# Kernel optimization log

Measured on AMD Instinct MI355X. Metric: run time of the kernel, lower is better.

The kernel has to match this reference:

```python
import jax, jax.numpy as jnp
import numpy as np

B, V, D, K, C_IN, C_OUT = 64, 2000, 16, 3, 64, 64


def setup_inputs() -> dict:
    key = jax.random.key(0)
    ks = jax.random.split(key, 7)
    return {
        "x": jax.random.normal(ks[0], (B, V, C_IN), dtype=jnp.float32),
        "ne_re": jax.random.normal(ks[1], (V, D), dtype=jnp.float32),
        "ne_im": jax.random.normal(ks[2], (V, D), dtype=jnp.float32),
        "w_re": jax.random.normal(ks[3], (D, K, C_IN, C_OUT), dtype=jnp.float32),
        "w_im": jax.random.normal(ks[4], (D, K, C_IN, C_OUT), dtype=jnp.float32),
        "b_re": jax.random.normal(ks[5], (D, C_OUT), dtype=jnp.float32),
        "b_im": jax.random.normal(ks[6], (D, C_OUT), dtype=jnp.float32),
    }


def reference(x, ne_re, ne_im, w_re, w_im, b_re, b_im):
    # Complex node embeddings and parameter pools (param_type='complex').
    ne = jax.lax.complex(ne_re, ne_im)                      # (V, D) complex64
    w_pool = jax.lax.complex(w_re, w_im)                    # (D, K, Ci, Co)
    b_pool = jax.lax.complex(b_re, b_im)                    # (D, Co)

    # Laplacian = E E^H, Frobenius-normalized (activation=None, normalization='frob').
    lap = ne @ ne.conj().T                                  # (V, V)
    lap = lap / jnp.linalg.norm(lap)

    # Node-adaptive weights and bias.
    weights = jnp.einsum('vd,dkio->vkio', ne, w_pool)       # (V, K, Ci, Co)
    bias = ne @ b_pool                                      # (V, Co)

    # Chebyshev-style recurrence, faithful to the source: T_k = 2*T_{k-1} - T_{k-2}
    # (the original code omits the laplacian matmul in the recurrence).
    polys = [jnp.eye(V, dtype=lap.dtype), lap]
    for k in range(2, K):
        polys.append(2.0 * polys[k - 1] - polys[k - 2])
    cheb = jnp.stack(polys, axis=0)                         # (K, V, V)

    xc = x.astype(lap.dtype)                                # (B, V, Ci)
    gx = jnp.einsum('kuv,bvi->buki', cheb, xc)              # (B, V, K, Ci)
    out = jnp.einsum('bvki,vkio->bvo', gx, weights) + bias  # (B, V, Co) complex

    # unwind=True path: view_as_real + flatten(2,3) -> interleaved (re, im).
    return jnp.stack([out.real, out.imag], axis=-1).reshape(B, V, 2 * C_OUT)
```

## Files before the change

### kernel.cpp

```cpp
#include <hip/hip_runtime.h>
#include <stdint.h>

#define BB 64
#define VV 2000
#define DD 16
#define CI 64
#define CO 64

#define WS_INV_DW   0
#define WS_GRAM_DW  8
#define WS_Z_DW     1024
#define WS_BIAS_DW  132096
#define WS_NE_B     1552384UL
#define WS_RHS_B    1814528UL
#define WS_U_B      4960256UL
#define WS_W_B      54112256UL
#define WS_ZP_DW    (WS_W_B / 4)

typedef __attribute__((ext_vector_type(8))) short short8;
typedef __attribute__((ext_vector_type(4))) float f32x4;

__device__ __forceinline__ uint32_t f2bf(float f) {
  uint32_t u = __float_as_uint(f);
  return (u + 0x7FFFu + ((u >> 16) & 1u)) >> 16;
}

__global__ void k_zero(float* __restrict__ ws) {
  reinterpret_cast<float4*>(ws)[threadIdx.x] = make_float4(0.f, 0.f, 0.f, 0.f);
}

__global__ void k_ne(const float* __restrict__ ne_re, const float* __restrict__ ne_im,
                     float* __restrict__ ws) {
  int gid = blockIdx.x * 256 + threadIdx.x;
  int u = gid >> 6, col = gid & 63;
  int h = col >> 5, kk = col & 31, d = kk >> 1, p = kk & 1;
  float v = 0.f;
  if (u < VV) v = p ? ne_im[u*DD + d] : ne_re[u*DD + d];
  uint32_t hi = f2bf(v);
  uint32_t ov = h ? f2bf(v - __uint_as_float(hi << 16)) : hi;
  ((uint16_t*)((char*)ws + WS_NE_B))[gid] = (uint16_t)ov;
}

__global__ void k_rhs(const float* __restrict__ w_re, const float* __restrict__ w_im,
                      float* __restrict__ ws) {
  int bx = blockIdx.x;
  int c = bx >> 4, ig4 = bx & 15;
  int t = threadIdx.x;
  int o = t & 63, il = t >> 6;
  int i = ig4*4 + il;
  int cb = c >> 1;
  int imf = c & 1;

  uint32_t row32[16];
  #pragma unroll
  for (int d = 0; d < DD; ++d) {
    int b0 = (d*192 + i)*64 + o;
    float vre, vim;
    if (cb == 0) {
      vre = w_re[b0] - w_re[b0 + 8192];
      vim = w_im[b0] - w_im[b0 + 8192];
    } else {
      vre = w_re[b0 + 4096] + 2.f*w_re[b0 + 8192];
      vim = w_im[b0 + 4096] + 2.f*w_im[b0 + 8192];
    }
    float q0 = imf ? vim : vre;
    float q1 = imf ? vre : -vim;
    row32[d] = f2bf(q0) | (f2bf(q1) << 16);
  }
  int s = ((i >> 3) ^ (o & 7)) & 7;
  int n = c*4096 + o*64 + s*8 + (i & 7);
  uint4* dst = (uint4*)((uint16_t*)((char*)ws + WS_RHS_B) + (size_t)n*64);
  #pragma unroll
  for (int j = 0; j < 4; ++j) {
    uint4 qv = make_uint4(row32[4*j], row32[4*j+1], row32[4*j+2], row32[4*j+3]);
    dst[j]     = qv;
    dst[j + 4] = qv;
  }
}

__global__ void k_norm1(const float* __restrict__ ne_re, const float* __restrict__ ne_im,
                        float* __restrict__ ws) {
  int t = threadIdx.x;
  int d = t >> 4, e = t & 15;
  int v0 = blockIdx.x * 80;
  float gr = 0.f, gi = 0.f;
  for (int v = v0; v < v0 + 80; ++v) {
    float ar = ne_re[v*DD + d], ai = ne_im[v*DD + d];
    float br = ne_re[v*DD + e], bi = ne_im[v*DD + e];
    gr += ar*br + ai*bi;
    gi += ar*bi - ai*br;
  }
  atomicAdd(ws + WS_GRAM_DW + 2*t,     gr);
  atomicAdd(ws + WS_GRAM_DW + 2*t + 1, gi);
}

__global__ void k_norm2(float* __restrict__ ws) {
  int t = threadIdx.x;
  float gr = ws[WS_GRAM_DW + 2*t], gi = ws[WS_GRAM_DW + 2*t + 1];
  __shared__ float red[256];
  red[t] = gr*gr + gi*gi;
  __syncthreads();
  for (int k = 128; k > 0; k >>= 1) {
    if (t < k) red[t] += red[t + k];
    __syncthreads();
  }
  if (t == 0) ws[WS_INV_DW] = 1.0f / sqrtf(red[0]);
}

__global__ void k_bias(const float* __restrict__ ne_re, const float* __restrict__ ne_im,
                       const float* __restrict__ b_re, const float* __restrict__ b_im,
                       float* __restrict__ ws) {
  int gid = blockIdx.x * 256 + threadIdx.x;
  int u = gid >> 7, idx = gid & 127;
  int o = idx >> 1, half = idx & 1;
  float acc = 0.f;
  #pragma unroll
  for (int d = 0; d < DD; ++d) {
    float nr = ne_re[u*DD + d], ni = ne_im[u*DD + d];
    float pr = b_re[d*CO + o],  pi = b_im[d*CO + o];
    acc += half ? (nr*pi + ni*pr) : (nr*pr - ni*pi);
  }
  ws[WS_BIAS_DW + gid] = acc;
}

__global__ void __launch_bounds__(256, 4)
k_z(const float* __restrict__ x, const float* __restrict__ ne_re,
    const float* __restrict__ ne_im, float* __restrict__ ws) {
  int b = blockIdx.x >> 4, c = blockIdx.x & 15;
  int t = threadIdx.x, lane = t & 63;
  int w = __builtin_amdgcn_readfirstlane(t >> 6);
  __shared__ __align__(16) float smem[8192];

  int vbase = c * 125;

  {
    const float4* xg = (const float4*)(x + ((size_t)b * VV + vbase) * CI);
    float4 rx[8];
    #pragma unroll
    for (int p = 0; p < 8; ++p) {
      int idx = p * 256 + t;
      if (idx < 2000) rx[p] = xg[idx];
    }
    #pragma unroll
    for (int p = 0; p < 8; ++p) {
      int idx = p * 256 + t;
      if (idx < 2000) *(float4*)&smem[idx * 4] = rx[p];
    }
  }
  __syncthreads();

  float zr[DD], zi[DD];
  #pragma unroll
  for (int d = 0; d < DD; ++d) { zr[d] = 0.f; zi[d] = 0.f; }

  int lv0 = (w * 125) >> 2;
  int lv1 = ((w + 1) * 125) >> 2;
  #pragma unroll 4
  for (int lv = lv0; lv < lv1; ++lv) {
    float xv = smem[lv * 64 + lane];
    int v = vbase + lv;
    #pragma unroll
    for (int d = 0; d < DD; ++d) {
      zr[d] += ne_re[v*DD + d] * xv;
      zi[d] -= ne_im[v*DD + d] * xv;
    }
  }
  __syncthreads();

  #pragma unroll
  for (int d = 0; d < DD; ++d) {
    smem[w*2048 + d*128 + lane*2 + 0] = zr[d];
    smem[w*2048 + d*128 + lane*2 + 1] = zi[d];
  }
  __syncthreads();
  float* ZP = ws + WS_ZP_DW;
  #pragma unroll
  for (int k = 0; k < 8; ++k) {
    int j = t + k*256;
    float s = smem[j] + smem[2048 + j] + smem[4096 + j] + smem[6144 + j];
    int d = j >> 7, r = j & 127;
    ZP[(size_t)c*131072 + d*8192 + b*128 + r] = s;
  }
}

__global__ void k_zred(float* __restrict__ ws) {
  int g = blockIdx.x * 256 + threadIdx.x;
  const float2* ZP2 = (const float2*)(ws + WS_ZP_DW);
  float2 acc = make_float2(0.f, 0.f);
  #pragma unroll
  for (int c = 0; c < 16; ++c) {
    float2 v = ZP2[(size_t)c*65536 + g];
    acc.x += v.x; acc.y += v.y;
  }
  ((float2*)(ws + WS_Z_DW))[g] = acc;
}

__global__ void __launch_bounds__(256, 4)
k_wgemm(float* __restrict__ ws) {
  const uint16_t* NE  = (const uint16_t*)((char*)ws + WS_NE_B);
  const uint16_t* RHS = (const uint16_t*)((char*)ws + WS_RHS_B);
  uint32_t*       W   = (uint32_t*)((char*)ws + WS_W_B);
  int ut = blockIdx.x, nc = blockIdx.y;
  int t = threadIdx.x, w = t >> 6, lane = t & 63;
  int n16 = lane & 15, quad = lane >> 4;
  short8 a[4][2];
  #pragma unroll
  for (int m = 0; m < 4; ++m) {
    int u = ut*64 + m*16 + n16;
    a[m][0] = *(const short8*)(NE + u*64 + quad*8);
    a[m][1] = *(const short8*)(NE + u*64 + 32 + quad*8);
  }
  int nbase = nc*1024 + w*256;
  #pragma unroll 2
  for (int pt = 0; pt < 8; ++pt) {
    int nb = nbase + pt*32;
    const uint16_t* r0 = RHS + (size_t)(nb + 2*n16 + 0)*64 + quad*8;
    const uint16_t* r1 = RHS + (size_t)(nb + 2*n16 + 1)*64 + quad*8;
    short8 b00 = *(const short8*)r0;
    short8 b01 = *(const short8*)(r0 + 32);
    short8 b10 = *(const short8*)r1;
    short8 b11 = *(const short8*)(r1 + 32);
    #pragma unroll
    for (int m = 0; m < 4; ++m) {
      f32x4 acc0 = (f32x4){0.f,0.f,0.f,0.f};
      f32x4 acc1 = (f32x4){0.f,0.f,0.f,0.f};
      acc0 = __builtin_amdgcn_mfma_f32_16x16x32_bf16(a[m][0], b00, acc0, 0, 0, 0);
      acc0 = __builtin_amdgcn_mfma_f32_16x16x32_bf16(a[m][1], b01, acc0, 0, 0, 0);
      acc1 = __builtin_amdgcn_mfma_f32_16x16x32_bf16(a[m][0], b10, acc1, 0, 0, 0);
      acc1 = __builtin_amdgcn_mfma_f32_16x16x32_bf16(a[m][1], b11, acc1, 0, 0, 0);
      #pragma unroll
      for (int r = 0; r < 4; ++r) {
        int u = ut*64 + m*16 + quad*4 + r;
        if (u < VV) {
          uint32_t pk = f2bf(acc0[r]) | (f2bf(acc1[r]) << 16);
          W[(size_t)u*8192 + (nb >> 1) + n16] = pk;
        }
      }
    }
  }
}

__global__ void __launch_bounds__(256, 4)
k_u(const float* __restrict__ x, const float* __restrict__ ne_re,
    const float* __restrict__ ne_im, float* __restrict__ ws) {
  int ug = blockIdx.x, by = blockIdx.y;
  int t = threadIdx.x, q = t >> 6, i = t & 63;
  int b = by*4 + q;
  float invn = ws[WS_INV_DW];

  float xv[16];
  {
    const float* xp = x + ((size_t)b*VV + (size_t)ug*16)*CI + i;
    #pragma unroll
    for (int ul = 0; ul < 16; ++ul) xv[ul] = xp[(size_t)ul*CI];
  }

  const float* Z = ws + WS_Z_DW;
  float zr[DD], zi[DD];
  #pragma unroll
  for (int d = 0; d < DD; ++d) {
    const float* zp = Z + (size_t)(d*4096 + b*64 + i) * 2;
    zr[d] = zp[0]; zi[d] = zp[1];
  }

  __shared__ uint16_t sStage[192 * 64];
  int bkey = b & 7;
  int pos = (((i >> 3) ^ bkey) & 7)*8 + (i & 7);

  #pragma unroll
  for (int ul = 0; ul < 16; ++ul)
    sStage[(ul*12 + 0 + q)*64 + pos] = (uint16_t)f2bf(xv[ul]);

  #pragma unroll
  for (int ul = 0; ul < 16; ++ul) {
    int u = ug*16 + ul;
    float yra = 0.f, yrb = 0.f, yia = 0.f, yib = 0.f;
    #pragma unroll
    for (int d = 0; d < DD; ++d) {
      float nr = ne_re[u*DD + d], ni = ne_im[u*DD + d];
      yra += nr*zr[d]; yrb += ni*zi[d];
      yia += nr*zi[d]; yib += ni*zr[d];
    }
    float yr = yra - yrb, yi = yia + yib;
    sStage[(ul*12 + 4 + q)*64 + pos] = (uint16_t)f2bf(yr * invn);
    sStage[(ul*12 + 8 + q)*64 + pos] = (uint16_t)f2bf(yi * invn);
  }
  __syncthreads();
  uint16_t* U = (uint16_t*)((char*)ws + WS_U_B);
  const uint4* sv = (const uint4*)sStage;
  #pragma unroll
  for (int pass = 0; pass < 6; ++pass) {
    int rr = pass*32 + (t >> 3), l8 = t & 7;
    int ul = rr / 12, rem = rr - ul*12;
    int c = rem >> 2, qq = rem & 3;
    uint4 v = sv[rr*8 + l8];
    *(uint4*)(U + (size_t)(ug*16 + ul)*12288 + c*4096 + (by*4 + qq)*64 + l8*8) = v;
  }
}

#define LP 80
#define CSTRIDE 5120
__global__ void __launch_bounds__(512, 2)
k_final(const float* __restrict__ ws, float* __restrict__ out) {
  int u = blockIdx.x, t = threadIdx.x;
  __shared__ __align__(16) uint16_t sW[4 * CSTRIDE];
  __shared__ __align__(16) uint16_t sU[3 * CSTRIDE];
  const uint4* Wg = (const uint4*)((const char*)ws + WS_W_B + (size_t)u*32768);
  const uint4* Ug = (const uint4*)((const char*)ws + WS_U_B + (size_t)u*24576);
  #pragma unroll
  for (int j = 0; j < 4; ++j) {
    int idx = j*512 + t;
    int row = idx >> 3, col = idx & 7;
    *(uint4*)&sW[row*LP + col*8] = Wg[idx];
  }
  #pragma unroll
  for (int j = 0; j < 3; ++j) {
    int idx = j*512 + t;
    int row = idx >> 3, col = idx & 7;
    *(uint4*)&sU[row*LP + col*8] = Ug[idx];
  }
  __syncthreads();

  int w = t >> 6, lane = t & 63;
  int n16 = lane & 15, quad = lane >> 4;
  int o = w*8 + (n16 >> 1), half = n16 & 1;
  int okey = o & 7;
  uint32_t sgnmask = half ? 0u : 0x80008000u;
  f32x4 acc[4];
  #pragma unroll
  for (int m = 0; m < 4; ++m) acc[m] = (f32x4){0.f,0.f,0.f,0.f};

  #pragma unroll
  for (int ks = 0; ks < 6; ++ks) {
    int cb = ks >> 1;
    int i8 = (ks & 1)*4 + quad;
    int c  = (cb == 0) ? half : ((cb == 1) ? 2 + half : 3 - half);
    int slot = (i8 ^ okey) & 7;
    short8 bfrag = *(const short8*)&sW[c*CSTRIDE + o*LP + slot*8];
    if (cb == 2) {
      uint32_t* bu = (uint32_t*)&bfrag;
      #pragma unroll
      for (int jj = 0; jj < 4; ++jj) bu[jj] ^= sgnmask;
    }
    #pragma unroll
    for (int m = 0; m < 4; ++m) {
      int b = m*16 + n16;
      int aslot = (i8 ^ (b & 7)) & 7;
      short8 afrag = *(const short8*)&sU[cb*CSTRIDE + b*LP + aslot*8];
      acc[m] = __builtin_amdgcn_mfma_f32_16x16x32_bf16(afrag, bfrag, acc[m], 0, 0, 0);
    }
  }

  float bias = ws[WS_BIAS_DW + u*128 + w*16 + n16];
  #pragma unroll
  for (int m = 0; m < 4; ++m) {
    #pragma unroll
    for (int r = 0; r < 4; ++r) {
      int b = m*16 + quad*4 + r;
      out[((size_t)b*VV + u)*128 + w*16 + n16] = acc[m][r] + bias;
    }
  }
}

extern "C" void kernel_launch(void* const* d_in, const int* in_sizes, int n_in,
                              void* d_out, int out_size, void* d_ws, size_t ws_size,
                              hipStream_t stream) {
  (void)in_sizes; (void)n_in; (void)out_size; (void)ws_size;
  const float* x     = (const float*)d_in[0];
  const float* ne_re = (const float*)d_in[1];
  const float* ne_im = (const float*)d_in[2];
  const float* w_re  = (const float*)d_in[3];
  const float* w_im  = (const float*)d_in[4];
  const float* b_re  = (const float*)d_in[5];
  const float* b_im  = (const float*)d_in[6];
  float* out = (float*)d_out;
  float* ws  = (float*)d_ws;

  k_zero <<<dim3(1),          dim3(256), 0, stream>>>(ws);
  k_ne   <<<dim3(512),        dim3(256), 0, stream>>>(ne_re, ne_im, ws);
  k_rhs  <<<dim3(64),         dim3(256), 0, stream>>>(w_re, w_im, ws);
  k_norm1<<<dim3(25),         dim3(256), 0, stream>>>(ne_re, ne_im, ws);
  k_norm2<<<dim3(1),          dim3(256), 0, stream>>>(ws);
  k_bias <<<dim3(1000),       dim3(256), 0, stream>>>(ne_re, ne_im, b_re, b_im, ws);
  k_z    <<<dim3(1024),       dim3(256), 0, stream>>>(x, ne_re, ne_im, ws);
  k_zred <<<dim3(256),        dim3(256), 0, stream>>>(ws);
  k_wgemm<<<dim3(32, 16),     dim3(256), 0, stream>>>(ws);
  k_u    <<<dim3(125, 16),    dim3(256), 0, stream>>>(x, ne_re, ne_im, ws);
  k_final<<<dim3(VV),         dim3(512), 0, stream>>>(ws, out);
}
```

Measured before the change: 219.2 us.

## Merge independent preprocessing kernels into two block-dispatched launches

The small setup kernels (z partials, ne packing, rhs packing, gram partials, bias) are fused into one launch that picks its role from the block index. The wgemm, z reduction and norm finalisation are fused into a second launch. This cuts the launch count from eleven to four and removes the zero-init kernel by replacing gram atomics with per-block partial sums. It also moves the z-partial buffer into the U region so it no longer overlaps the W output written in the same launch. The cost is a larger shared-memory footprint per block, because the z body's 32KB array now applies to every block in the merged kernel, which may reduce occupancy for the lighter roles.

```diff
diff --git a/kernel.cpp b/kernel.cpp
--- a/kernel.cpp
+++ b/kernel.cpp
@@ -8,14 +8,14 @@
 #define CO 64
 
 #define WS_INV_DW   0
-#define WS_GRAM_DW  8
 #define WS_Z_DW     1024
 #define WS_BIAS_DW  132096
 #define WS_NE_B     1552384UL
 #define WS_RHS_B    1814528UL
 #define WS_U_B      4960256UL
 #define WS_W_B      54112256UL
-#define WS_ZP_DW    (WS_W_B / 4)
+#define WS_ZP_DW    (WS_U_B / 4)
+#define WS_NP_DW    (WS_ZP_DW + 2097152)
 
 typedef __attribute__((ext_vector_type(8))) short short8;
 typedef __attribute__((ext_vector_type(4))) float f32x4;
@@ -25,13 +25,71 @@
   return (u + 0x7FFFu + ((u >> 16) & 1u)) >> 16;
 }
 
-__global__ void k_zero(float* __restrict__ ws) {
-  reinterpret_cast<float4*>(ws)[threadIdx.x] = make_float4(0.f, 0.f, 0.f, 0.f);
-}
-
-__global__ void k_ne(const float* __restrict__ ne_re, const float* __restrict__ ne_im,
-                     float* __restrict__ ws) {
-  int gid = blockIdx.x * 256 + threadIdx.x;
+
+__device__ __forceinline__ void body_z(int bz, int t,
+    const float* __restrict__ x, const float* __restrict__ ne_re,
+    const float* __restrict__ ne_im, float* __restrict__ ws) {
+  int b = bz >> 4, c = bz & 15;
+  int lane = t & 63;
+  int w = __builtin_amdgcn_readfirstlane(t >> 6);
+  __shared__ __align__(16) float smem[8192];
+
+  int vbase = c * 125;
+
+  {
+    const float4* xg = (const float4*)(x + ((size_t)b * VV + vbase) * CI);
+    float4 rx[8];
+    #pragma unroll
+    for (int p = 0; p < 8; ++p) {
+      int idx = p * 256 + t;
+      if (idx < 2000) rx[p] = xg[idx];
+    }
+    #pragma unroll
+    for (int p = 0; p < 8; ++p) {
+      int idx = p * 256 + t;
+      if (idx < 2000) *(float4*)&smem[idx * 4] = rx[p];
+    }
+  }
+  __syncthreads();
+
+  float zr[DD], zi[DD];
+  #pragma unroll
+  for (int d = 0; d < DD; ++d) { zr[d] = 0.f; zi[d] = 0.f; }
+
+  int lv0 = (w * 125) >> 2;
+  int lv1 = ((w + 1) * 125) >> 2;
+  #pragma unroll 4
+  for (int lv = lv0; lv < lv1; ++lv) {
+    float xv = smem[lv * 64 + lane];
+    int v = vbase + lv;
+    #pragma unroll
+    for (int d = 0; d < DD; ++d) {
+      zr[d] += ne_re[v*DD + d] * xv;
+      zi[d] -= ne_im[v*DD + d] * xv;
+    }
+  }
+  __syncthreads();
+
+  #pragma unroll
+  for (int d = 0; d < DD; ++d) {
+    smem[w*2048 + d*128 + lane*2 + 0] = zr[d];
+    smem[w*2048 + d*128 + lane*2 + 1] = zi[d];
+  }
+  __syncthreads();
+  float* ZP = ws + WS_ZP_DW;
+  #pragma unroll
+  for (int k = 0; k < 8; ++k) {
+    int j = t + k*256;
+    float s = smem[j] + smem[2048 + j] + smem[4096 + j] + smem[6144 + j];
+    int d = j >> 7, r = j & 127;
+    ZP[(size_t)c*131072 + d*8192 + b*128 + r] = s;
+  }
+}
+
+__device__ __forceinline__ void body_ne(int bx, int t,
+    const float* __restrict__ ne_re, const float* __restrict__ ne_im,
+    float* __restrict__ ws) {
+  int gid = bx * 256 + t;
   int u = gid >> 6, col = gid & 63;
   int h = col >> 5, kk = col & 31, d = kk >> 1, p = kk & 1;
   float v = 0.f;
@@ -41,11 +99,10 @@
   ((uint16_t*)((char*)ws + WS_NE_B))[gid] = (uint16_t)ov;
 }
 
-__global__ void k_rhs(const float* __restrict__ w_re, const float* __restrict__ w_im,
-                      float* __restrict__ ws) {
-  int bx = blockIdx.x;
+__device__ __forceinline__ void body_rhs(int bx, int t,
+    const float* __restrict__ w_re, const float* __restrict__ w_im,
+    float* __restrict__ ws) {
   int c = bx >> 4, ig4 = bx & 15;
-  int t = threadIdx.x;
   int o = t & 63, il = t >> 6;
   int i = ig4*4 + il;
   int cb = c >> 1;
@@ -78,11 +135,11 @@
   }
 }
 
-__global__ void k_norm1(const float* __restrict__ ne_re, const float* __restrict__ ne_im,
-                        float* __restrict__ ws) {
-  int t = threadIdx.x;
+__device__ __forceinline__ void body_norm1(int bx, int t,
+    const float* __restrict__ ne_re, const float* __restrict__ ne_im,
+    float* __restrict__ ws) {
   int d = t >> 4, e = t & 15;
-  int v0 = blockIdx.x * 80;
+  int v0 = bx * 80;
   float gr = 0.f, gi = 0.f;
   for (int v = v0; v < v0 + 80; ++v) {
     float ar = ne_re[v*DD + d], ai = ne_im[v*DD + d];
@@ -90,27 +147,16 @@
     gr += ar*br + ai*bi;
     gi += ar*bi - ai*br;
   }
-  atomicAdd(ws + WS_GRAM_DW + 2*t,     gr);
-  atomicAdd(ws + WS_GRAM_DW + 2*t + 1, gi);
-}
-
-__global__ void k_norm2(float* __restrict__ ws) {
-  int t = threadIdx.x;
-  float gr = ws[WS_GRAM_DW + 2*t], gi = ws[WS_GRAM_DW + 2*t + 1];
-  __shared__ float red[256];
-  red[t] = gr*gr + gi*gi;
-  __syncthreads();
-  for (int k = 128; k > 0; k >>= 1) {
-    if (t < k) red[t] += red[t + k];
-    __syncthreads();
-  }
-  if (t == 0) ws[WS_INV_DW] = 1.0f / sqrtf(red[0]);
-}
-
-__global__ void k_bias(const float* __restrict__ ne_re, const float* __restrict__ ne_im,
-                       const float* __restrict__ b_re, const float* __restrict__ b_im,
-                       float* __restrict__ ws) {
-  int gid = blockIdx.x * 256 + threadIdx.x;
+  float* NP = ws + WS_NP_DW;
+  NP[bx*512 + 2*t]     = gr;
+  NP[bx*512 + 2*t + 1] = gi;
+}
+
+__device__ __forceinline__ void body_bias(int bx, int t,
+    const float* __restrict__ ne_re, const float* __restrict__ ne_im,
+    const float* __restrict__ b_re, const float* __restrict__ b_im,
+    float* __restrict__ ws) {
+  int gid = bx * 256 + t;
   int u = gid >> 7, idx = gid & 127;
   int o = idx >> 1, half = idx & 1;
   float acc = 0.f;
@@ -123,85 +169,12 @@
   ws[WS_BIAS_DW + gid] = acc;
 }
 
-__global__ void __launch_bounds__(256, 4)
-k_z(const float* __restrict__ x, const float* __restrict__ ne_re,
-    const float* __restrict__ ne_im, float* __restrict__ ws) {
-  int b = blockIdx.x >> 4, c = blockIdx.x & 15;
-  int t = threadIdx.x, lane = t & 63;
-  int w = __builtin_amdgcn_readfirstlane(t >> 6);
-  __shared__ __align__(16) float smem[8192];
-
-  int vbase = c * 125;
-
-  {
-    const float4* xg = (const float4*)(x + ((size_t)b * VV + vbase) * CI);
-    float4 rx[8];
-    #pragma unroll
-    for (int p = 0; p < 8; ++p) {
-      int idx = p * 256 + t;
-      if (idx < 2000) rx[p] = xg[idx];
-    }
-    #pragma unroll
-    for (int p = 0; p < 8; ++p) {
-      int idx = p * 256 + t;
-      if (idx < 2000) *(float4*)&smem[idx * 4] = rx[p];
-    }
-  }
-  __syncthreads();
-
-  float zr[DD], zi[DD];
-  #pragma unroll
-  for (int d = 0; d < DD; ++d) { zr[d] = 0.f; zi[d] = 0.f; }
-
-  int lv0 = (w * 125) >> 2;
-  int lv1 = ((w + 1) * 125) >> 2;
-  #pragma unroll 4
-  for (int lv = lv0; lv < lv1; ++lv) {
-    float xv = smem[lv * 64 + lane];
-    int v = vbase + lv;
-    #pragma unroll
-    for (int d = 0; d < DD; ++d) {
-      zr[d] += ne_re[v*DD + d] * xv;
-      zi[d] -= ne_im[v*DD + d] * xv;
-    }
-  }
-  __syncthreads();
-
-  #pragma unroll
-  for (int d = 0; d < DD; ++d) {
-    smem[w*2048 + d*128 + lane*2 + 0] = zr[d];
-    smem[w*2048 + d*128 + lane*2 + 1] = zi[d];
-  }
-  __syncthreads();
-  float* ZP = ws + WS_ZP_DW;
-  #pragma unroll
-  for (int k = 0; k < 8; ++k) {
-    int j = t + k*256;
-    float s = smem[j] + smem[2048 + j] + smem[4096 + j] + smem[6144 + j];
-    int d = j >> 7, r = j & 127;
-    ZP[(size_t)c*131072 + d*8192 + b*128 + r] = s;
-  }
-}
-
-__global__ void k_zred(float* __restrict__ ws) {
-  int g = blockIdx.x * 256 + threadIdx.x;
-  const float2* ZP2 = (const float2*)(ws + WS_ZP_DW);
-  float2 acc = make_float2(0.f, 0.f);
-  #pragma unroll
-  for (int c = 0; c < 16; ++c) {
-    float2 v = ZP2[(size_t)c*65536 + g];
-    acc.x += v.x; acc.y += v.y;
-  }
-  ((float2*)(ws + WS_Z_DW))[g] = acc;
-}
-
-__global__ void __launch_bounds__(256, 4)
-k_wgemm(float* __restrict__ ws) {
+__device__ __forceinline__ void body_wgemm(int bx, int t, float* __restrict__ ws) {
   const uint16_t* NE  = (const uint16_t*)((char*)ws + WS_NE_B);
   const uint16_t* RHS = (const uint16_t*)((char*)ws + WS_RHS_B);
   uint32_t*       W   = (uint32_t*)((char*)ws + WS_W_B);
-  int ut = blockIdx.x, nc = blockIdx.y;
-  int t = threadIdx.x, w = t >> 6, lane = t & 63;
+  int ut = bx & 31, nc = bx >> 5;
+  int w = t >> 6, lane = t & 63;
   int n16 = lane & 15, quad = lane >> 4;
   short8 a[4][2];
   #pragma unroll
@@ -240,6 +213,68 @@
   }
 }
 
+__device__ __forceinline__ void body_zred(int bx, int t, float* __restrict__ ws) {
+  int g = bx * 256 + t;
+  const float2* ZP2 = (const float2*)(ws + WS_ZP_DW);
+  float2 acc = make_float2(0.f, 0.f);
+  #pragma unroll
+  for (int c = 0; c < 16; ++c) {
+    float2 v = ZP2[(size_t)c*65536 + g];
+    acc.x += v.x; acc.y += v.y;
+  }
+  ((float2*)(ws + WS_Z_DW))[g] = acc;
+}
+
+__device__ __forceinline__ void body_norm2(int t, float* __restrict__ ws) {
+  const float* NP = ws + WS_NP_DW;
+  float gr = 0.f, gi = 0.f;
+  #pragma unroll
+  for (int p = 0; p < 25; ++p) {
+    gr += NP[p*512 + 2*t];
+    gi += NP[p*512 + 2*t + 1];
+  }
+  __shared__ float red[256];
+  red[t] = gr*gr + gi*gi;
+  __syncthreads();
+  for (int k = 128; k > 0; k >>= 1) {
+    if (t < k) red[t] += red[t + k];
+    __syncthreads();
+  }
+  if (t == 0) ws[WS_INV_DW] = 1.0f / sqrtf(red[0]);
+}
+
+
+__global__ void __launch_bounds__(256, 4)
+k_front(const float* __restrict__ x, const float* __restrict__ ne_re,
+        const float* __restrict__ ne_im, const float* __restrict__ w_re,
+        const float* __restrict__ w_im, const float* __restrict__ b_re,
+        const float* __restrict__ b_im, float* __restrict__ ws) {
+  int bx = blockIdx.x, t = threadIdx.x;
+  if (bx < 1024) {
+    body_z(bx, t, x, ne_re, ne_im, ws);
+  } else if (bx < 1536) {
+    body_ne(bx - 1024, t, ne_re, ne_im, ws);
+  } else if (bx < 1600) {
+    body_rhs(bx - 1536, t, w_re, w_im, ws);
+  } else if (bx < 1625) {
+    body_norm1(bx - 1600, t, ne_re, ne_im, ws);
+  } else {
+    body_bias(bx - 1625, t, ne_re, ne_im, b_re, b_im, ws);
+  }
+}
+
+__global__ void __launch_bounds__(256, 4)
+k_mid(float* __restrict__ ws) {
+  int bx = blockIdx.x, t = threadIdx.x;
+  if (bx < 512) {
+    body_wgemm(bx, t, ws);
+  } else if (bx < 768) {
+    body_zred(bx - 512, t, ws);
+  } else {
+    body_norm2(t, ws);
+  }
+}
+
 __global__ void __launch_bounds__(256, 4)
 k_u(const float* __restrict__ x, const float* __restrict__ ne_re,
     const float* __restrict__ ne_im, float* __restrict__ ws) {
@@ -376,15 +411,9 @@
   float* out = (float*)d_out;
   float* ws  = (float*)d_ws;
 
-  k_zero <<<dim3(1),          dim3(256), 0, stream>>>(ws);
-  k_ne   <<<dim3(512),        dim3(256), 0, stream>>>(ne_re, ne_im, ws);
-  k_rhs  <<<dim3(64),         dim3(256), 0, stream>>>(w_re, w_im, ws);
-  k_norm1<<<dim3(25),         dim3(256), 0, stream>>>(ne_re, ne_im, ws);
-  k_norm2<<<dim3(1),          dim3(256), 0, stream>>>(ws);
-  k_bias <<<dim3(1000),       dim3(256), 0, stream>>>(ne_re, ne_im, b_re, b_im, ws);
-  k_z    <<<dim3(1024),       dim3(256), 0, stream>>>(x, ne_re, ne_im, ws);
-  k_zred <<<dim3(256),        dim3(256), 0, stream>>>(ws);
-  k_wgemm<<<dim3(32, 16),     dim3(256), 0, stream>>>(ws);
-  k_u    <<<dim3(125, 16),    dim3(256), 0, stream>>>(x, ne_re, ne_im, ws);
-  k_final<<<dim3(VV),         dim3(512), 0, stream>>>(ws, out);
-}
+  k_front<<<dim3(2625),    dim3(256), 0, stream>>>(x, ne_re, ne_im, w_re, w_im,
+                                                   b_re, b_im, ws);
+  k_mid  <<<dim3(769),     dim3(256), 0, stream>>>(ws);
+  k_u    <<<dim3(125, 16), dim3(256), 0, stream>>>(x, ne_re, ne_im, ws);
+  k_final<<<dim3(VV),      dim3(512), 0, stream>>>(ws, out);
+}
```

Result: faster. 198.0 us (-9.7%).
